# Optimization experiments

Hardware: AMD Instinct MI355X
Metric: run time of the kernel (lower is better)

The kernel has to match this reference:

```python
import jax, jax.numpy as jnp
import numpy as np

B, C, H, W = 8, 1152, 32, 32
N = H * W


def _skew(t):
    # t: (B,3) -> (B,3,3) skew-symmetric
    z = jnp.zeros_like(t[:, 0])
    return jnp.stack([
        jnp.stack([z, -t[:, 2], t[:, 1]], axis=-1),
        jnp.stack([t[:, 2], z, -t[:, 0]], axis=-1),
        jnp.stack([-t[:, 1], t[:, 0], z], axis=-1),
    ], axis=1)


def _fundamental(K1, K2, R, t):
    E = _skew(t) @ R
    U, S, Vt = jnp.linalg.svd(E)
    S = S.at[:, 2].set(0.0)  # enforce rank-2 essential matrix
    E = U @ (S[:, :, None] * Vt)
    return jnp.linalg.inv(jnp.swapaxes(K2, 1, 2)) @ E @ jnp.linalg.inv(K1)


def setup_inputs() -> dict:
    key = jax.random.key(0)
    k1, k2, k3, k4, k5 = jax.random.split(key, 5)
    f_tar = jax.random.normal(k1, (B, C, H, W), dtype=jnp.float32)
    f_src = jax.random.normal(k2, (B, C, H, W), dtype=jnp.float32)
    # realistic invertible intrinsics: [[fx,0,cx],[0,fy,cy],[0,0,1]]
    def intrinsics(k):
        f = 30.0 + 2.0 * jax.random.uniform(k, (B, 2))
        Kt = jnp.zeros((B, 3, 3))
        Kt = Kt.at[:, 0, 0].set(f[:, 0]).at[:, 1, 1].set(f[:, 1])
        Kt = Kt.at[:, 0, 2].set(W / 2.0).at[:, 1, 2].set(H / 2.0).at[:, 2, 2].set(1.0)
        return Kt.astype(jnp.float32)
    K1 = intrinsics(k3)
    K2 = intrinsics(k4)
    # proper rotation via QR of a random matrix
    ka, kb = jax.random.split(k5)
    Q, Rm = jnp.linalg.qr(jax.random.normal(ka, (B, 3, 3)))
    Q = Q * jnp.sign(jnp.diagonal(Rm, axis1=1, axis2=2))[:, None, :]
    Q = Q * jnp.linalg.det(Q)[:, None, None]  # det = +1
    t = jax.random.normal(kb, (B, 3), dtype=jnp.float32)
    return {"f_tar": f_tar, "f_src": f_src, "K1": K1, "K2": K2,
            "R": Q.astype(jnp.float32), "t": t}


def reference(f_tar, f_src, K1, K2, R, t):
    f_src_flat = f_src.reshape(B, C, N)  # (B,C,N)
    # NOTE: torch code computes A = f_src^T @ f_tar but never uses it (dead code); omitted.

    # homogeneous pixel coords, indexing='ij': x=row index, y=col index
    ix, iy = jnp.meshgrid(jnp.arange(H, dtype=jnp.float32),
                          jnp.arange(W, dtype=jnp.float32), indexing='ij')
    combined = jnp.stack([ix.ravel(), iy.ravel(), jnp.ones(N, jnp.float32)], axis=0)  # (3,N)
    combined = jnp.broadcast_to(combined, (B, 3, N))

    F_mat = _fundamental(K1, K2, R, t)                       # (B,3,3)
    lines = F_mat @ combined                                 # (B,3,N)
    lines = lines / lines[:, 2:3, :]

    ones = jnp.ones((B, 1, N), jnp.float32)
    x0 = jnp.zeros((B, 1, N), jnp.float32)
    y0 = -lines[:, 2:3, :] / lines[:, 1:2, :]
    point_0 = jnp.concatenate([x0, y0, ones], axis=1)        # (B,3,N)
    x1 = jnp.full((B, 1, N), float(W), jnp.float32)
    y1 = -(lines[:, 2:3, :] + lines[:, 0:1, :] * W) / lines[:, 1:2, :]
    point_1 = jnp.concatenate([x1, y1, ones], axis=1)        # (B,3,N)

    # point-to-line distance for every (pixel i, line j) pair -> (B,N,N)
    diff = point_0 - point_1                                 # (B,3,N)
    p = combined[:, :, :, None] - point_0[:, :, None, :]     # (B,3,N,N) via broadcast
    d = diff[:, :, None, :]                                  # (B,3,1,N)
    cross = jnp.stack([
        p[:, 1] * d[:, 2] - p[:, 2] * d[:, 1],
        p[:, 2] * d[:, 0] - p[:, 0] * d[:, 2],
        p[:, 0] * d[:, 1] - p[:, 1] * d[:, 0],
    ], axis=1)                                               # (B,3,N,N)
    cross_norm = jnp.sqrt(jnp.sum(cross * cross, axis=1))    # (B,N,N)
    diff_norm = jnp.linalg.norm(diff, axis=1, keepdims=True) # (B,1,N)
    d_epi = cross_norm / diff_norm                           # (B,N,N)

    thre = 0.1
    weight_map = 1.0 - jax.nn.softmax(5.0 * (d_epi - thre), axis=-1)
    attention_map = jax.nn.softmax(weight_map, axis=1)       # softmax over dim=1, per torch code

    out = jnp.einsum('bij,bjc->bic', attention_map, jnp.swapaxes(f_src_flat, 1, 2))  # (B,N,C)
    return out.reshape(B, C, H, W)
```

## Files before the change

### kernel.cpp

```cpp
#include <hip/hip_runtime.h>
#include <hip/hip_bf16.h>
#include <math.h>

#define Bn 8
#define Cn 1152
#define Nn 1024

typedef short short8 __attribute__((ext_vector_type(8)));
typedef float f32x4 __attribute__((ext_vector_type(4)));

__device__ float g_csum_part[Bn * 32 * Nn];
__device__ unsigned short g_A[(size_t)Bn * Nn * Nn];
__device__ unsigned short g_fb[(size_t)Bn * Cn * Nn];

__device__ inline unsigned short f2bf(float x) {
    __hip_bfloat16 h = __float2bfloat16(x);
    unsigned short u;
    __builtin_memcpy(&u, &h, 2);
    return u;
}

__device__ inline void inv3(const float* M, float* o) {
    float a = M[0], b = M[1], c = M[2];
    float d = M[3], e = M[4], f = M[5];
    float g = M[6], h = M[7], i = M[8];
    float A0 = (e * i - f * h);
    float A1 = -(d * i - f * g);
    float A2 = (d * h - e * g);
    float det = a * A0 + b * A1 + c * A2;
    float inv = 1.0f / det;
    o[0] = A0 * inv;
    o[1] = -(b * i - c * h) * inv;
    o[2] = (b * f - c * e) * inv;
    o[3] = A1 * inv;
    o[4] = (a * i - c * g) * inv;
    o[5] = -(a * f - c * d) * inv;
    o[6] = A2 * inv;
    o[7] = -(a * h - b * g) * inv;
    o[8] = (a * e - b * d) * inv;
}

__device__ inline void mm3(const float* X, const float* Y, float* Z) {
    for (int r = 0; r < 3; r++)
        for (int c = 0; c < 3; c++)
            Z[r * 3 + c] = X[r * 3 + 0] * Y[0 * 3 + c] + X[r * 3 + 1] * Y[1 * 3 + c] +
                           X[r * 3 + 2] * Y[2 * 3 + c];
}

__device__ inline void computeF(const float* K1, const float* K2, const float* R,
                                const float* t, int b, float* F) {
    float t0 = t[b * 3 + 0], t1 = t[b * 3 + 1], t2 = t[b * 3 + 2];
    float S[9] = {0.0f, -t2, t1, t2, 0.0f, -t0, -t1, t0, 0.0f};
    float E[9];
    mm3(S, &R[b * 9], E);
    float iK1[9], iK2[9];
    inv3(&K1[b * 9], iK1);
    inv3(&K2[b * 9], iK2);
    float iK2T[9] = {iK2[0], iK2[3], iK2[6], iK2[1], iK2[4], iK2[7], iK2[2], iK2[5], iK2[8]};
    float T[9];
    mm3(iK2T, E, T);
    mm3(T, iK1, F);
}

__device__ inline float4 zcoef(const float* F, int j) {
    float jx = (float)(j >> 5);
    float jy = (float)(j & 31);
    float l0 = F[0] * jx + F[1] * jy + F[2];
    float l1 = F[3] * jx + F[4] * jy + F[5];
    float l2 = F[6] * jx + F[7] * jy + F[8];
    l0 = l0 / l2;
    l1 = l1 / l2;
    float y0 = -1.0f / l1;
    float y1 = -(1.0f + l0 * 32.0f) / l1;
    float dy = y0 - y1;
    float invn = 1.0f / sqrtf(1024.0f + dy * dy);
    return make_float4(5.0f * dy * invn, 160.0f * invn, 160.0f * y0 * invn, 0.0f);
}

__launch_bounds__(256) __global__ void fusedE_kernel(const float* __restrict__ K1,
                                                     const float* __restrict__ K2,
                                                     const float* __restrict__ R,
                                                     const float* __restrict__ t) {
    __shared__ float Fs[9];
    __shared__ float4 prm[Nn];
    __shared__ float red[4][16][64];
    int lin = blockIdx.x;
    int b = lin & 7;
    int seg = lin >> 3;
    if (threadIdx.x == 0) computeF(K1, K2, R, t, b, Fs);
    __syncthreads();
#pragma unroll
    for (int u = 0; u < 4; u++) {
        int j = threadIdx.x * 4 + u;
        prm[j] = zcoef(Fs, j);
    }
    __syncthreads();
    int wv = threadIdx.x >> 6;
    int lane = threadIdx.x & 63;
    float px[16], py[16], pz[16];
#pragma unroll
    for (int k = 0; k < 16; k++) {
        float4 p = prm[lane + k * 64];
        px[k] = p.x;
        py[k] = p.y;
        pz[k] = p.z;
    }
    float csum[16];
#pragma unroll
    for (int k = 0; k < 16; k++) csum[k] = 0.0f;
#pragma unroll
    for (int rr = 0; rr < 8; rr++) {
        int i = seg * 32 + wv * 8 + rr;
        float ix = (float)(i >> 5), iy = (float)(i & 31);
        float e[16], m = -INFINITY;
#pragma unroll
        for (int k = 0; k < 16; k++) {
            e[k] = fabsf(fmaf(ix, px[k], fmaf(iy, py[k], -pz[k]))) - 0.5f;
            m = fmaxf(m, e[k]);
        }
#pragma unroll
        for (int o = 32; o > 0; o >>= 1) m = fmaxf(m, __shfl_xor(m, o, 64));
        float s = 0.0f;
#pragma unroll
        for (int k = 0; k < 16; k++) {
            e[k] = __expf(e[k] - m);
            s += e[k];
        }
#pragma unroll
        for (int o = 32; o > 0; o >>= 1) s += __shfl_xor(s, o, 64);
        float rsi = 1.0f / s;
        unsigned short* arow = g_A + (size_t)(b * Nn + i) * Nn;
#pragma unroll
        for (int k = 0; k < 16; k++) {
            float E = __expf(1.0f - e[k] * rsi);
            csum[k] += E;
            arow[lane + k * 64] = f2bf(E);
        }
    }
#pragma unroll
    for (int k = 0; k < 16; k++) red[wv][k][lane] = csum[k];
    __syncthreads();
    int l2 = threadIdx.x & 63;
    int k0 = (threadIdx.x >> 6) * 4;
#pragma unroll
    for (int q = 0; q < 4; q++) {
        int k = k0 + q;
        float ssum = red[0][k][l2] + red[1][k][l2] + red[2][k][l2] + red[3][k][l2];
        g_csum_part[(b * 32 + seg) * Nn + k * 64 + l2] = ssum;
    }
}

__global__ void convert_fsrc_kernel(const float* __restrict__ f) {
    int lin = blockIdx.x;
    int b = lin & 7;
    int cg = lin >> 3;
    int j0 = threadIdx.x * 4;
    float4 cs = *(const float4*)&g_csum_part[(b * 32 + 0) * Nn + j0];
#pragma unroll
    for (int it = 1; it < 32; it++) {
        float4 p = *(const float4*)&g_csum_part[(b * 32 + it) * Nn + j0];
        cs.x += p.x; cs.y += p.y; cs.z += p.z; cs.w += p.w;
    }
    float4 inv = make_float4(1.0f / cs.x, 1.0f / cs.y, 1.0f / cs.z, 1.0f / cs.w);
#pragma unroll
    for (int c8 = 0; c8 < 8; c8++) {
        int c = cg * 8 + c8;
        size_t off = ((size_t)b * Cn + c) * Nn + j0;
        float4 v = *(const float4*)(f + off);
        ushort4 u;
        u.x = f2bf(v.x * inv.x);
        u.y = f2bf(v.y * inv.y);
        u.z = f2bf(v.z * inv.z);
        u.w = f2bf(v.w * inv.w);
        *(ushort4*)&g_fb[off] = u;
    }
}

#define BM 128
#define BNc 64
#define BK 32
#define NSTEP (Nn / BK)

__launch_bounds__(128) __global__ void gemm_kernel(float* __restrict__ out) {
    __shared__ unsigned short As[4][BM * BK];
    __shared__ unsigned short Bs[4][BNc * BK];
    int lin = blockIdx.x;
    int b = lin & 7;
    int s = lin >> 3;
    int it = s & 7;
    int ct = s >> 3;
    int i0 = it * BM;
    int c0 = ct * BNc;
    int t = threadIdx.x;
    int w = t >> 6, L = t & 63;
    const unsigned short* Ab = g_A + (size_t)b * Nn * Nn + (size_t)i0 * Nn;
    const unsigned short* Fb = g_fb + (size_t)b * Cn * Nn + (size_t)c0 * Nn;

    auto stage = [&](int p, int kt) {
#pragma unroll
        for (int h = 0; h < 4; h++) {
            int chunk = h * 128 + t;
            int rr = chunk >> 2;
            int gq = (chunk & 3) ^ ((rr >> 1) & 3);
            const unsigned short* ga = Ab + (size_t)rr * Nn + kt + gq * 8;
            __builtin_amdgcn_global_load_lds(
                (const __attribute__((address_space(1))) unsigned int*)ga,
                (__attribute__((address_space(3))) unsigned int*)(As[p] + chunk * 8), 16, 0, 0);
        }
#pragma unroll
        for (int h = 0; h < 2; h++) {
            int chunk = h * 128 + t;
            int rr = chunk >> 2;
            int gq = (chunk & 3) ^ ((rr >> 1) & 3);
            const unsigned short* gb = Fb + (size_t)rr * Nn + kt + gq * 8;
            __builtin_amdgcn_global_load_lds(
                (const __attribute__((address_space(1))) unsigned int*)gb,
                (__attribute__((address_space(3))) unsigned int*)(Bs[p] + chunk * 8), 16, 0, 0);
        }
    };

    f32x4 acc[4][4] = {};
    int lrow = L & 15, quad = L >> 4;
    stage(0, 0);
    stage(1, BK);
    stage(2, 2 * BK);
    for (int st = 0; st < NSTEP; ++st) {
        if (st < NSTEP - 2) {
            asm volatile("s_waitcnt vmcnt(12)\n\ts_barrier" ::: "memory");
        } else if (st == NSTEP - 2) {
            asm volatile("s_waitcnt vmcnt(6)\n\ts_barrier" ::: "memory");
        } else {
            asm volatile("s_waitcnt vmcnt(0)\n\ts_barrier" ::: "memory");
        }
        if (st + 3 < NSTEP) stage((st + 3) & 3, (st + 3) * BK);
        int p = st & 3;
        short8 af[4], bf[4];
#pragma unroll
        for (int mt = 0; mt < 4; mt++) {
            int rr = w * 64 + mt * 16 + lrow;
            int q = quad ^ ((rr >> 1) & 3);
            af[mt] = *(const short8*)(As[p] + rr * BK + q * 8);
        }
#pragma unroll
        for (int nt = 0; nt < 4; nt++) {
            int cc = nt * 16 + lrow;
            int q = quad ^ ((cc >> 1) & 3);
            bf[nt] = *(const short8*)(Bs[p] + cc * BK + q * 8);
        }
#pragma unroll
        for (int mt = 0; mt < 4; mt++)
#pragma unroll
            for (int nt = 0; nt < 4; nt++)
                acc[mt][nt] =
                    __builtin_amdgcn_mfma_f32_16x16x32_bf16(af[mt], bf[nt], acc[mt][nt], 0, 0, 0);
    }
    int col = L & 15;
#pragma unroll
    for (int mt = 0; mt < 4; mt++)
#pragma unroll
        for (int rg = 0; rg < 4; rg++) {
            int i = i0 + w * 64 + mt * 16 + quad * 4 + rg;
            float* orow = out + ((size_t)b * Nn + i) * Cn + c0;
#pragma unroll
            for (int nt = 0; nt < 4; nt++) orow[nt * 16 + col] = acc[mt][nt][rg];
        }
}

extern "C" void kernel_launch(void* const* d_in, const int* in_sizes, int n_in,
                              void* d_out, int out_size, void* d_ws, size_t ws_size,
                              hipStream_t stream) {
    (void)in_sizes; (void)n_in; (void)d_ws; (void)ws_size; (void)out_size;
    const float* f_src = (const float*)d_in[1];
    const float* K1 = (const float*)d_in[2];
    const float* K2 = (const float*)d_in[3];
    const float* R = (const float*)d_in[4];
    const float* t = (const float*)d_in[5];
    float* out = (float*)d_out;

    fusedE_kernel<<<dim3(256), dim3(256), 0, stream>>>(K1, K2, R, t);
    convert_fsrc_kernel<<<dim3(Bn * Cn / 8), dim3(256), 0, stream>>>(f_src);
    gemm_kernel<<<dim3(Bn * (Nn / BM) * (Cn / BNc)), dim3(128), 0, stream>>>(out);
}
```

Measured before the change: 181.9 us.

## Replace async LDS-direct 4-stage pipeline with register-staged double buffering

The GEMM's four-stage pipeline of direct global-to-LDS loads with manual vmcnt waits is replaced by a two-buffer scheme. The next K-tile is loaded into registers before the MFMA loop and written to the other LDS buffer afterwards. Per-thread global pointers are precomputed once, and launch bounds now request two blocks per SIMD. Shared memory drops by half, which may raise occupancy. The trade-off is fewer tiles in flight and extra registers plus explicit LDS write instructions.

```diff
diff --git a/kernel.cpp b/kernel.cpp
--- a/kernel.cpp
+++ b/kernel.cpp
@@ -181,9 +181,9 @@
 #define BK 32
 #define NSTEP (Nn / BK)
 
-__launch_bounds__(128) __global__ void gemm_kernel(float* __restrict__ out) {
-    __shared__ unsigned short As[4][BM * BK];
-    __shared__ unsigned short Bs[4][BNc * BK];
+__launch_bounds__(128, 2) __global__ void gemm_kernel(float* __restrict__ out) {
+    __shared__ unsigned short As[2][BM * BK];
+    __shared__ unsigned short Bs[2][BNc * BK];
     int lin = blockIdx.x;
     int b = lin & 7;
     int s = lin >> 3;
@@ -196,44 +196,53 @@
     const unsigned short* Ab = g_A + (size_t)b * Nn * Nn + (size_t)i0 * Nn;
     const unsigned short* Fb = g_fb + (size_t)b * Cn * Nn + (size_t)c0 * Nn;
 
-    auto stage = [&](int p, int kt) {
-#pragma unroll
-        for (int h = 0; h < 4; h++) {
-            int chunk = h * 128 + t;
-            int rr = chunk >> 2;
-            int gq = (chunk & 3) ^ ((rr >> 1) & 3);
-            const unsigned short* ga = Ab + (size_t)rr * Nn + kt + gq * 8;
-            __builtin_amdgcn_global_load_lds(
-                (const __attribute__((address_space(1))) unsigned int*)ga,
-                (__attribute__((address_space(3))) unsigned int*)(As[p] + chunk * 8), 16, 0, 0);
-        }
-#pragma unroll
-        for (int h = 0; h < 2; h++) {
-            int chunk = h * 128 + t;
-            int rr = chunk >> 2;
-            int gq = (chunk & 3) ^ ((rr >> 1) & 3);
-            const unsigned short* gb = Fb + (size_t)rr * Nn + kt + gq * 8;
-            __builtin_amdgcn_global_load_lds(
-                (const __attribute__((address_space(1))) unsigned int*)gb,
-                (__attribute__((address_space(3))) unsigned int*)(Bs[p] + chunk * 8), 16, 0, 0);
-        }
+    const unsigned short* pa[4];
+    int oa[4];
+#pragma unroll
+    for (int h = 0; h < 4; h++) {
+        int chunk = h * 128 + t;
+        int rr = chunk >> 2;
+        int gq = (chunk & 3) ^ ((rr >> 1) & 3);
+        pa[h] = Ab + (size_t)rr * Nn + gq * 8;
+        oa[h] = chunk * 8;
+    }
+    const unsigned short* pb[2];
+    int ob[2];
+#pragma unroll
+    for (int h = 0; h < 2; h++) {
+        int chunk = h * 128 + t;
+        int rr = chunk >> 2;
+        int gq = (chunk & 3) ^ ((rr >> 1) & 3);
+        pb[h] = Fb + (size_t)rr * Nn + gq * 8;
+        ob[h] = chunk * 8;
+    }
+
+    short8 la0, la1, la2, la3, lb0, lb1;
+    auto loadRegs = [&](int kt) {
+        la0 = *(const short8*)(pa[0] + kt);
+        la1 = *(const short8*)(pa[1] + kt);
+        la2 = *(const short8*)(pa[2] + kt);
+        la3 = *(const short8*)(pa[3] + kt);
+        lb0 = *(const short8*)(pb[0] + kt);
+        lb1 = *(const short8*)(pb[1] + kt);
+    };
+    auto writeRegs = [&](int q) {
+        *(short8*)(As[q] + oa[0]) = la0;
+        *(short8*)(As[q] + oa[1]) = la1;
+        *(short8*)(As[q] + oa[2]) = la2;
+        *(short8*)(As[q] + oa[3]) = la3;
+        *(short8*)(Bs[q] + ob[0]) = lb0;
+        *(short8*)(Bs[q] + ob[1]) = lb1;
     };
 
     f32x4 acc[4][4] = {};
     int lrow = L & 15, quad = L >> 4;
-    stage(0, 0);
-    stage(1, BK);
-    stage(2, 2 * BK);
+    loadRegs(0);
+    writeRegs(0);
     for (int st = 0; st < NSTEP; ++st) {
-        if (st < NSTEP - 2) {
-            asm volatile("s_waitcnt vmcnt(12)\n\ts_barrier" ::: "memory");
-        } else if (st == NSTEP - 2) {
-            asm volatile("s_waitcnt vmcnt(6)\n\ts_barrier" ::: "memory");
-        } else {
-            asm volatile("s_waitcnt vmcnt(0)\n\ts_barrier" ::: "memory");
-        }
-        if (st + 3 < NSTEP) stage((st + 3) & 3, (st + 3) * BK);
-        int p = st & 3;
+        __syncthreads();
+        int p = st & 1;
+        if (st + 1 < NSTEP) loadRegs((st + 1) * BK);
         short8 af[4], bf[4];
 #pragma unroll
         for (int mt = 0; mt < 4; mt++) {
@@ -253,6 +262,7 @@
             for (int nt = 0; nt < 4; nt++)
                 acc[mt][nt] =
                     __builtin_amdgcn_mfma_f32_16x16x32_bf16(af[mt], bf[nt], acc[mt][nt], 0, 0, 0);
+        if (st + 1 < NSTEP) writeRegs(1 - p);
     }
     int col = L & 15;
 #pragma unroll
```

After: 172.0 us. -5.4%, faster.
